# Optimization experiments

Hardware: AMD Instinct MI355X
Metric: run time of the kernel (lower is better)

Reference implementation:

```python
import jax, jax.numpy as jnp
import numpy as np

N = 100000        # num nodes
E2 = 3200000      # num directed edges (symmetric)
D = 256           # node feature dim
C = 40            # num classes
NIDS = 1000       # labelled node ids
TOL = 0.01
MAXITER = 16
AVG_DEG = E2 // N // 2 * 2  # ~32


def setup_inputs() -> dict:
    key = jax.random.key(0)
    k1, k2, k3, k4, k5, k6 = jax.random.split(key, 6)
    E = E2 // 2
    row_h = jax.random.randint(k1, (E,), 0, N, dtype=jnp.int32)
    col_h = jax.random.randint(k2, (E,), 0, N, dtype=jnp.int32)
    # symmetrize so I - (1-eps)*A is SPD-like (CG assumption)
    row = jnp.concatenate([row_h, col_h])
    col = jnp.concatenate([col_h, row_h])
    vals = jax.random.uniform(k3, (E,), dtype=jnp.float32) * (0.9 / 32.0)
    data = jnp.concatenate([vals, vals])
    node_features = jax.random.normal(k4, (N, D), dtype=jnp.float32)
    ids = jax.random.randint(k5, (NIDS,), 0, N, dtype=jnp.int32)
    # hk.Linear with TruncatedNormal(stddev=1/sqrt(D)) init
    W = (jax.random.truncated_normal(k6, -2.0, 2.0, (D, C), dtype=jnp.float32)
         * (1.0 / np.sqrt(D))).astype(jnp.float32)
    b = jnp.zeros((C,), jnp.float32)
    e0 = jnp.zeros((), jnp.float32)  # hk.get_parameter('e0', (), init=zeros)
    return dict(node_features=node_features, W=W, b=b, e0=e0,
                data=data, row=row, col=col, ids=ids)


def reference(node_features, W, b, e0, data, row, col, ids):
    epsilon = jax.nn.sigmoid(e0)
    # head_transform=None; d_feat > num_classes -> Linear first, then smooth
    x = node_features @ W + b  # [N, C]

    def spmv(v):  # adj @ v for COO adjacency, v: [N, C]
        return jax.ops.segment_sum(data[:, None] * v[col], row, num_segments=N)

    def f(v):  # (I - (1-eps) A) v
        return v - (1.0 - epsilon) * spmv(v)

    # smooth(): x.shape[1] (=C) <= ids.size -> direct CG on dense x, then gather ids
    sol, _ = jax.scipy.sparse.linalg.cg(f, x, tol=TOL, maxiter=MAXITER)
    return sol[ids]  # [NIDS, C] logits
```

## Files before the change

kernel.cpp:

```cpp
#include <hip/hip_runtime.h>
#include <hip/hip_fp16.h>
#include <math.h>

#define NNODE  100000
#define NEDGE  3200000
#define DFEAT  256
#define NCLS   40
#define NC_TOT 4000000
#define NIDS   1000
#define TOLSQ  1.0e-4f
#define MAXIT  16

#define SB 2048
#define SLOT8 500000
#define SPB8 245
#define XB 1024
#define VT 256
#define GR     128
#define GEMM_B 782

#define RB      128
#define NBUCK   782
#define BCAP    6144
#define SUBB    1024
#define NPB     800
#define EPB     4000

__device__ __forceinline__ float block_reduce_256(float v, float* red) {
  int tid = threadIdx.x;
  red[tid] = v;
  __syncthreads();
  #pragma unroll
  for (int off = 128; off > 0; off >>= 1) {
    if (tid < off) red[tid] += red[tid + off];
    __syncthreads();
  }
  float res = red[0];
  __syncthreads();
  return res;
}

__global__ void __launch_bounds__(256) k_pcount(const int* __restrict__ row,
                                                int* __restrict__ cntmat,
                                                int* __restrict__ total) {
  __shared__ int h[NBUCK];
  int tid = threadIdx.x, blk = blockIdx.x;
  for (int i = tid; i < NBUCK; i += 256) h[i] = 0;
  __syncthreads();
  int e0 = blk * EPB;
  for (int i = tid; i < EPB; i += 256) atomicAdd(&h[row[e0 + i] >> 7], 1);
  __syncthreads();
  for (int i = tid; i < NBUCK; i += 256) {
    int v = h[i];
    cntmat[blk * NBUCK + i] = v;
    if (v) atomicAdd(&total[i], v);
  }
}

__global__ void k_bscan2(const int* __restrict__ total, int* __restrict__ bptr) {
  __shared__ int s[1024];
  int tid = threadIdx.x;
  int v = (tid < NBUCK) ? total[tid] : 0;
  s[tid] = v;
  __syncthreads();
  for (int off = 1; off < 1024; off <<= 1) {
    int t = (tid >= off) ? s[tid - off] : 0;
    __syncthreads();
    s[tid] += t;
    __syncthreads();
  }
  if (tid < NBUCK) bptr[tid] = s[tid] - v;
  if (tid == 0) bptr[NBUCK] = NEDGE;
}

__global__ void __launch_bounds__(1024) k_colscan(int* __restrict__ cntmat,
                                                  const int* __restrict__ bptr) {
  __shared__ int s[1024];
  int b = blockIdx.x;
  int tid = threadIdx.x;
  int v = (tid < NPB) ? cntmat[tid * NBUCK + b] : 0;
  s[tid] = v;
  __syncthreads();
  for (int off = 1; off < 1024; off <<= 1) {
    int t = (tid >= off) ? s[tid - off] : 0;
    __syncthreads();
    s[tid] += t;
    __syncthreads();
  }
  if (tid < NPB) cntmat[tid * NBUCK + b] = bptr[b] + s[tid] - v;
}

__global__ void __launch_bounds__(512) k_ppart(const int* __restrict__ row,
    const int* __restrict__ col, const float* __restrict__ data,
    const int* __restrict__ offmat, uint2* __restrict__ bstage) {
  __shared__ int cnt[NBUCK];
  __shared__ int segs[NBUCK + 1];
  __shared__ int cur[NBUCK];
  __shared__ int goff[NBUCK];
  __shared__ int scp[512];
  __shared__ unsigned short bof[EPB];
  __shared__ uint2 pay[EPB];
  int tid = threadIdx.x, blk = blockIdx.x;
  int e0 = blk * EPB;

  for (int i = tid; i < NBUCK; i += 512) {
    cnt[i] = 0;
    goff[i] = offmat[blk * NBUCK + i];
  }
  __syncthreads();
  for (int i = tid; i < EPB; i += 512) atomicAdd(&cnt[row[e0 + i] >> 7], 1);
  __syncthreads();

  int t2 = tid * 2;
  int l0 = (t2 + 0 < NBUCK) ? cnt[t2 + 0] : 0;
  int l1 = (t2 + 1 < NBUCK) ? cnt[t2 + 1] : 0;
  int mysum = l0 + l1;
  scp[tid] = mysum;
  __syncthreads();
  for (int off = 1; off < 512; off <<= 1) {
    int t = (tid >= off) ? scp[tid - off] : 0;
    __syncthreads();
    scp[tid] += t;
    __syncthreads();
  }
  int base = scp[tid] - mysum;
  if (t2 + 0 <= NBUCK) segs[t2 + 0] = base;  base += l0;
  if (t2 + 1 <= NBUCK) segs[t2 + 1] = base;
  for (int i = tid; i < NBUCK; i += 512) cur[i] = 0;
  __syncthreads();

  for (int b = tid; b < NBUCK; b += 512) {
    int s1 = segs[b + 1];
    for (int i = segs[b]; i < s1; ++i) bof[i] = (unsigned short)b;
  }
  for (int i = tid; i < EPB; i += 512) {
    int rr = row[e0 + i];
    int b = rr >> 7;
    int rk = atomicAdd(&cur[b], 1);
    pay[segs[b] + rk] = make_uint2(((unsigned)(rr & (RB - 1)) << 17) | (unsigned)col[e0 + i],
                                   __float_as_uint(data[e0 + i]));
  }
  __syncthreads();
  for (int i = tid; i < EPB; i += 512) {
    int b = bof[i];
    bstage[goff[b] + (i - segs[b])] = pay[i];
  }
}

__global__ void __launch_bounds__(512) k_bbuild(const int* __restrict__ bptr,
    const uint2* __restrict__ bstage, int* __restrict__ rowptr,
    int2* __restrict__ csr) {
  __shared__ uint2 ebuf[BCAP];
  __shared__ int deg[SUBB];
  __shared__ int segs[SUBB];
  __shared__ int scp[512];
  int b = blockIdx.x;
  int s0 = bptr[b], s1 = bptr[b + 1];
  int n = s1 - s0;
  if (n > BCAP) n = BCAP;
  int tid = threadIdx.x;
  for (int i = tid; i < SUBB; i += 512) deg[i] = 0;
  __syncthreads();
  for (int i = tid; i < n; i += 512) {
    uint2 e = bstage[s0 + i];
    ebuf[i] = e;
    int key = (int)(e.x >> 17) * 8 + (int)((e.x & 0x1FFFF) >> 14);
    atomicAdd(&deg[key], 1);
  }
  __syncthreads();
  int t2 = tid * 2;
  int l0 = deg[t2 + 0], l1 = deg[t2 + 1];
  int mysum = l0 + l1;
  scp[tid] = mysum;
  __syncthreads();
  for (int off = 1; off < 512; off <<= 1) {
    int t = (tid >= off) ? scp[tid - off] : 0;
    __syncthreads();
    scp[tid] += t;
    __syncthreads();
  }
  int base = scp[tid] - mysum;
  segs[t2 + 0] = base;  base += l0;
  segs[t2 + 1] = base;
  __syncthreads();
  for (int i = tid; i < SUBB; i += 512) deg[i] = 0;
  if (tid < RB) {
    int grow = b * RB + tid;
    if (grow < NNODE) rowptr[grow] = s0 + segs[tid * 8];
  }
  if (b == 0 && tid == 0) rowptr[NNODE] = NEDGE;
  __syncthreads();
  for (int i = tid; i < n; i += 512) {
    uint2 e = ebuf[i];
    int col = (int)(e.x & 0x1FFFF);
    int key = (int)(e.x >> 17) * 8 + (col >> 14);
    int pos = atomicAdd(&deg[key], 1);
    csr[s0 + segs[key] + pos] = make_int2(col, (int)e.y);
  }
}

__global__ void __launch_bounds__(256) k_gemm(const float* __restrict__ feat,
    const float* __restrict__ W, const float* __restrict__ bias,
    float* __restrict__ r, float* __restrict__ p, __half* __restrict__ ph,
    float* __restrict__ part) {
  __shared__ float wtile[DFEAT * NCLS];
  __shared__ float red[256];
  int tid = threadIdx.x;
  int r0 = blockIdx.x * GR;
  int rl0 = (tid >> 2) * 2;
  int cbase = (tid & 3) * 10;
  float acc0[10], acc1[10];
  #pragma unroll
  for (int j = 0; j < 10; ++j) {
    float bv = bias[cbase + j];
    acc0[j] = bv;
    acc1[j] = bv;
  }

  #pragma unroll
  for (int it = 0; it < DFEAT * NCLS / 256; ++it)
    wtile[tid + it * 256] = W[tid + it * 256];
  __syncthreads();

  int g0 = r0 + rl0, g1 = g0 + 1;
  int g0c = (g0 < NNODE) ? g0 : NNODE - 1;
  int g1c = (g1 < NNODE) ? g1 : NNODE - 1;
  const float* f0p = feat + (size_t)g0c * DFEAT;
  const float* f1p = feat + (size_t)g1c * DFEAT;

  #pragma unroll 4
  for (int kq = 0; kq < DFEAT / 4; ++kq) {
    float4 f0 = *(const float4*)(f0p + kq * 4);
    float4 f1 = *(const float4*)(f1p + kq * 4);
    const float* w0 = &wtile[(kq * 4 + 0) * NCLS + cbase];
    const float* w1 = &wtile[(kq * 4 + 1) * NCLS + cbase];
    const float* w2 = &wtile[(kq * 4 + 2) * NCLS + cbase];
    const float* w3 = &wtile[(kq * 4 + 3) * NCLS + cbase];
    #pragma unroll
    for (int j = 0; j < 10; ++j) {
      float wa = w0[j], wb = w1[j], wc = w2[j], wd = w3[j];
      acc0[j] = fmaf(f0.x, wa, acc0[j]);
      acc0[j] = fmaf(f0.y, wb, acc0[j]);
      acc0[j] = fmaf(f0.z, wc, acc0[j]);
      acc0[j] = fmaf(f0.w, wd, acc0[j]);
      acc1[j] = fmaf(f1.x, wa, acc1[j]);
      acc1[j] = fmaf(f1.y, wb, acc1[j]);
      acc1[j] = fmaf(f1.z, wc, acc1[j]);
      acc1[j] = fmaf(f1.w, wd, acc1[j]);
    }
  }

  float local = 0.f;
  if (g0 < NNODE) {
    size_t b0 = (size_t)g0 * NCLS + cbase;
    #pragma unroll
    for (int j = 0; j < 10; ++j) {
      float a = acc0[j];
      r[b0 + j] = a; p[b0 + j] = a; ph[b0 + j] = __float2half(a);
      local = fmaf(a, a, local);
    }
  }
  if (g1 < NNODE) {
    size_t b1 = (size_t)g1 * NCLS + cbase;
    #pragma unroll
    for (int j = 0; j < 10; ++j) {
      float a = acc1[j];
      r[b1 + j] = a; p[b1 + j] = a; ph[b1 + j] = __float2half(a);
      local = fmaf(a, a, local);
    }
  }
  float tot = block_reduce_256(local, red);
  if (tid == 0) part[blockIdx.x] = tot;
}

__global__ void k_init_scal(const float* __restrict__ part, const float* __restrict__ e0,
                            float* __restrict__ scal) {
  __shared__ float red[256];
  float local = 0.f;
  for (int i = threadIdx.x; i < GEMM_B; i += 256) local += part[i];
  float bs = block_reduce_256(local, red);
  if (threadIdx.x == 0) {
    float eps = 1.f / (1.f + expf(-e0[0]));
    scal[0] = 1.f - eps;
    scal[1] = TOLSQ * bs;
    scal[2] = bs;
  }
}

__global__ void __launch_bounds__(VT) k_spmv(const float* __restrict__ scal, int k,
    const int* __restrict__ rowptr, const int2* __restrict__ csr,
    const __half* __restrict__ ph, const float* __restrict__ p,
    float* __restrict__ Ap, float* __restrict__ part) {
  float gamma = scal[2 + k], atol2 = scal[1];
  if (!(gamma > atol2)) return;
  float omega = scal[0];
  int b = blockIdx.x;
  int chunk = (b & 7) * (SB / 8) + (b >> 3);
  int sbase = chunk * SPB8;
  float local = 0.f;
  int li = threadIdx.x;
  int s = sbase + li;
  if (li < SPB8 && s < SLOT8) {
    int rr = s / 5;
    int c8 = (s - rr * 5) * 8;
    int s0 = rowptr[rr], s1 = rowptr[rr + 1];
    float a0 = 0.f, a1 = 0.f, a2 = 0.f, a3 = 0.f;
    float a4 = 0.f, a5 = 0.f, a6 = 0.f, a7 = 0.f;
    #pragma unroll 4
    for (int j = s0; j < s1; ++j) {
      int2 pr = csr[j];
      float w = __int_as_float(pr.y);
      uint4 g = *(const uint4*)(ph + (size_t)pr.x * NCLS + c8);
      float2 f01 = __half22float2(*(__half2*)&g.x);
      float2 f23 = __half22float2(*(__half2*)&g.y);
      float2 f45 = __half22float2(*(__half2*)&g.z);
      float2 f67 = __half22float2(*(__half2*)&g.w);
      a0 = fmaf(w, f01.x, a0); a1 = fmaf(w, f01.y, a1);
      a2 = fmaf(w, f23.x, a2); a3 = fmaf(w, f23.y, a3);
      a4 = fmaf(w, f45.x, a4); a5 = fmaf(w, f45.y, a5);
      a6 = fmaf(w, f67.x, a6); a7 = fmaf(w, f67.y, a7);
    }
    size_t e = (size_t)rr * NCLS + c8;
    float4 pe0 = *(const float4*)(p + e);
    float4 pe1 = *(const float4*)(p + e + 4);
    float4 v0, v1;
    v0.x = fmaf(-omega, a0, pe0.x); v0.y = fmaf(-omega, a1, pe0.y);
    v0.z = fmaf(-omega, a2, pe0.z); v0.w = fmaf(-omega, a3, pe0.w);
    v1.x = fmaf(-omega, a4, pe1.x); v1.y = fmaf(-omega, a5, pe1.y);
    v1.z = fmaf(-omega, a6, pe1.z); v1.w = fmaf(-omega, a7, pe1.w);
    *(float4*)(Ap + e) = v0;
    *(float4*)(Ap + e + 4) = v1;
    local = fmaf(pe0.x, v0.x, local); local = fmaf(pe0.y, v0.y, local);
    local = fmaf(pe0.z, v0.z, local); local = fmaf(pe0.w, v0.w, local);
    local = fmaf(pe1.x, v1.x, local); local = fmaf(pe1.y, v1.y, local);
    local = fmaf(pe1.z, v1.z, local); local = fmaf(pe1.w, v1.w, local);
  }
  __shared__ float red[256];
  float tot = block_reduce_256(local, red);
  if (threadIdx.x == 0) part[blockIdx.x] = tot;
}

__global__ void __launch_bounds__(VT) k_xr(const float* __restrict__ scal, int k,
    const float* __restrict__ part_in,
    const float* __restrict__ p, const float* __restrict__ Ap,
    float* __restrict__ r, const int* __restrict__ ids,
    float* __restrict__ out, float* __restrict__ part_out) {
  float gamma = scal[2 + k], atol2 = scal[1];
  if (!(gamma > atol2)) return;
  __shared__ float red[256];
  float lp = 0.f;
  for (int i = threadIdx.x; i < SB; i += VT) lp += part_in[i];
  float pap = block_reduce_256(lp, red);
  float alpha = gamma / pap;
  int idx = blockIdx.x * VT + threadIdx.x;
  if (idx < NIDS * NCLS) {
    int i = idx / NCLS, c = idx - (idx / NCLS) * NCLS;
    out[idx] += alpha * p[(size_t)ids[i] * NCLS + c];
  }
  const float4* a4 = (const float4*)Ap;
  float4* r4 = (float4*)r;
  float local = 0.f;
  int stride = gridDim.x * blockDim.x;
  for (int e = blockIdx.x * blockDim.x + threadIdx.x; e < NC_TOT / 4; e += stride) {
    float4 ae = a4[e], re = r4[e];
    re.x = fmaf(-alpha, ae.x, re.x); re.y = fmaf(-alpha, ae.y, re.y);
    re.z = fmaf(-alpha, ae.z, re.z); re.w = fmaf(-alpha, ae.w, re.w);
    r4[e] = re;
    local = fmaf(re.x, re.x, local); local = fmaf(re.y, re.y, local);
    local = fmaf(re.z, re.z, local); local = fmaf(re.w, re.w, local);
  }
  float tot = block_reduce_256(local, red);
  if (threadIdx.x == 0) part_out[blockIdx.x] = tot;
}

__global__ void __launch_bounds__(VT) k_pupd(float* __restrict__ scal, int k,
    const float* __restrict__ part_in,
    const float* __restrict__ r, float* __restrict__ p, __half* __restrict__ ph) {
  float gamma = scal[2 + k], atol2 = scal[1];
  if (!(gamma > atol2)) {
    if (blockIdx.x == 0 && threadIdx.x == 0) scal[2 + k + 1] = gamma;
    return;
  }
  __shared__ float red[256];
  float lp = 0.f;
  for (int i = threadIdx.x; i < XB; i += VT) lp += part_in[i];
  float gnew = block_reduce_256(lp, red);
  float beta = gnew / gamma;
  const float4* r4 = (const float4*)r;
  float4* p4 = (float4*)p;
  int stride = gridDim.x * blockDim.x;
  for (int e = blockIdx.x * blockDim.x + threadIdx.x; e < NC_TOT / 4; e += stride) {
    float4 pe = p4[e], re = r4[e];
    pe.x = fmaf(beta, pe.x, re.x); pe.y = fmaf(beta, pe.y, re.y);
    pe.z = fmaf(beta, pe.z, re.z); pe.w = fmaf(beta, pe.w, re.w);
    p4[e] = pe;
    int e4 = e * 4;
    ph[e4 + 0] = __float2half(pe.x);
    ph[e4 + 1] = __float2half(pe.y);
    ph[e4 + 2] = __float2half(pe.z);
    ph[e4 + 3] = __float2half(pe.w);
  }
  if (blockIdx.x == 0 && threadIdx.x == 0) scal[2 + k + 1] = gnew;
}

extern "C" void kernel_launch(void* const* d_in, const int* in_sizes, int n_in,
                              void* d_out, int out_size, void* d_ws, size_t ws_size,
                              hipStream_t stream) {
  const float* feat = (const float*)d_in[0];
  const float* W    = (const float*)d_in[1];
  const float* bias = (const float*)d_in[2];
  const float* e0   = (const float*)d_in[3];
  const float* data = (const float*)d_in[4];
  const int*   row  = (const int*)d_in[5];
  const int*   col  = (const int*)d_in[6];
  const int*   ids  = (const int*)d_in[7];
  float* out = (float*)d_out;

  size_t off = 0;
  char* base = (char*)d_ws;
  auto take = [&](size_t nbytes) -> void* {
    void* ptr = base + off;
    off += (nbytes + 255) & ~(size_t)255;
    return ptr;
  };
  float* rv  = (float*)take((size_t)NC_TOT * 4);
  float* pv  = (float*)take((size_t)NC_TOT * 4);
  float* ap  = (float*)take((size_t)NC_TOT * 4);
  __half* ph = (__half*)take((size_t)NC_TOT * 2);
  int2*  csr = (int2*)take((size_t)NEDGE * 8);
  int* rowptr    = (int*)take((size_t)(NNODE + 1) * 4);
  int* cntmat    = (int*)take((size_t)NPB * NBUCK * 4);
  int* total     = (int*)take((size_t)(NBUCK + 2) * 4);
  int* bptr      = (int*)take((size_t)(NBUCK + 2) * 4);
  float* part_a  = (float*)take(SB * 4);
  float* part_b  = (float*)take(XB * 4);
  float* scal    = (float*)take(64 * 4);

  uint2* bstage = (uint2*)rv;

  hipMemsetAsync(total, 0, (size_t)(NBUCK + 2) * 4, stream);
  hipMemsetAsync(out, 0, (size_t)NIDS * NCLS * 4, stream);
  k_pcount<<<NPB, 256, 0, stream>>>(row, cntmat, total);
  k_bscan2<<<1, 1024, 0, stream>>>(total, bptr);
  k_colscan<<<NBUCK, 1024, 0, stream>>>(cntmat, bptr);
  k_ppart<<<NPB, 512, 0, stream>>>(row, col, data, cntmat, bstage);
  k_bbuild<<<NBUCK, 512, 0, stream>>>(bptr, bstage, rowptr, csr);

  k_gemm<<<GEMM_B, 256, 0, stream>>>(feat, W, bias, rv, pv, ph, part_a);
  k_init_scal<<<1, 256, 0, stream>>>(part_a, e0, scal);

  for (int k = 0; k < MAXIT; ++k) {
    k_spmv<<<SB, VT, 0, stream>>>(scal, k, rowptr, csr, ph, pv, ap, part_a);
    k_xr  <<<XB, VT, 0, stream>>>(scal, k, part_a, pv, ap, rv, ids, out, part_b);
    k_pupd<<<XB, VT, 0, stream>>>(scal, k, part_b, rv, pv, ph);
  }
}
```

Measured before the change: 389.7 us.

## Split GEMM reduction dimension across two blocks and combine in a separate kernel

The feature-projection GEMM now splits the 256-wide reduction into two halves handled by separate blocks. This doubles the grid and halves the shared W tile, which should raise occupancy. A new combine kernel adds the two partial results, writes r, p and the half-precision p, and computes the initial residual norm partials. The cost is an extra 16MB partial buffer and an additional kernel pass over 4M-element arrays.

```diff
diff --git a/kernel.cpp b/kernel.cpp
--- a/kernel.cpp
+++ b/kernel.cpp
@@ -18,6 +18,8 @@
 #define VT 256
 #define GR     128
 #define GEMM_B 782
+#define GEMM_B2 1564
+#define KHALF  128
 
 #define RB      128
 #define NBUCK   782
@@ -201,35 +203,35 @@
 
 __global__ void __launch_bounds__(256) k_gemm(const float* __restrict__ feat,
     const float* __restrict__ W, const float* __restrict__ bias,
-    float* __restrict__ r, float* __restrict__ p, __half* __restrict__ ph,
-    float* __restrict__ part) {
-  __shared__ float wtile[DFEAT * NCLS];
-  __shared__ float red[256];
+    float* __restrict__ pb0, float* __restrict__ pb1) {
+  __shared__ float wtile[KHALF * NCLS];
   int tid = threadIdx.x;
-  int r0 = blockIdx.x * GR;
+  int b = blockIdx.x;
+  int half = b & 1;
+  int r0 = (b >> 1) * GR;
   int rl0 = (tid >> 2) * 2;
   int cbase = (tid & 3) * 10;
   float acc0[10], acc1[10];
   #pragma unroll
   for (int j = 0; j < 10; ++j) {
-    float bv = bias[cbase + j];
+    float bv = half ? 0.f : bias[cbase + j];
     acc0[j] = bv;
     acc1[j] = bv;
   }
 
   #pragma unroll
-  for (int it = 0; it < DFEAT * NCLS / 256; ++it)
-    wtile[tid + it * 256] = W[tid + it * 256];
+  for (int it = 0; it < KHALF * NCLS / 256; ++it)
+    wtile[tid + it * 256] = W[half * KHALF * NCLS + tid + it * 256];
   __syncthreads();
 
   int g0 = r0 + rl0, g1 = g0 + 1;
   int g0c = (g0 < NNODE) ? g0 : NNODE - 1;
   int g1c = (g1 < NNODE) ? g1 : NNODE - 1;
-  const float* f0p = feat + (size_t)g0c * DFEAT;
-  const float* f1p = feat + (size_t)g1c * DFEAT;
+  const float* f0p = feat + (size_t)g0c * DFEAT + half * KHALF;
+  const float* f1p = feat + (size_t)g1c * DFEAT + half * KHALF;
 
   #pragma unroll 4
-  for (int kq = 0; kq < DFEAT / 4; ++kq) {
+  for (int kq = 0; kq < KHALF / 4; ++kq) {
     float4 f0 = *(const float4*)(f0p + kq * 4);
     float4 f1 = *(const float4*)(f1p + kq * 4);
     const float* w0 = &wtile[(kq * 4 + 0) * NCLS + cbase];
@@ -250,34 +252,52 @@
     }
   }
 
-  float local = 0.f;
+  float* __restrict__ pb = half ? pb1 : pb0;
   if (g0 < NNODE) {
     size_t b0 = (size_t)g0 * NCLS + cbase;
     #pragma unroll
-    for (int j = 0; j < 10; ++j) {
-      float a = acc0[j];
-      r[b0 + j] = a; p[b0 + j] = a; ph[b0 + j] = __float2half(a);
-      local = fmaf(a, a, local);
-    }
+    for (int j = 0; j < 10; ++j) pb[b0 + j] = acc0[j];
   }
   if (g1 < NNODE) {
     size_t b1 = (size_t)g1 * NCLS + cbase;
     #pragma unroll
-    for (int j = 0; j < 10; ++j) {
-      float a = acc1[j];
-      r[b1 + j] = a; p[b1 + j] = a; ph[b1 + j] = __float2half(a);
-      local = fmaf(a, a, local);
-    }
+    for (int j = 0; j < 10; ++j) pb[b1 + j] = acc1[j];
+  }
+}
+
+__global__ void __launch_bounds__(VT) k_gcomb(const float* __restrict__ pb0,
+    const float* __restrict__ pb1, float* __restrict__ r, float* __restrict__ p,
+    __half* __restrict__ ph, float* __restrict__ part) {
+  __shared__ float red[256];
+  const float4* a4 = (const float4*)pb0;
+  const float4* b4 = (const float4*)pb1;
+  float4* r4 = (float4*)r;
+  float4* p4 = (float4*)p;
+  float local = 0.f;
+  int stride = gridDim.x * blockDim.x;
+  for (int e = blockIdx.x * blockDim.x + threadIdx.x; e < NC_TOT / 4; e += stride) {
+    float4 a = a4[e], b = b4[e];
+    float4 v;
+    v.x = a.x + b.x; v.y = a.y + b.y; v.z = a.z + b.z; v.w = a.w + b.w;
+    r4[e] = v; p4[e] = v;
+    __half2 h01 = __floats2half2_rn(v.x, v.y);
+    __half2 h23 = __floats2half2_rn(v.z, v.w);
+    uint2 pack;
+    pack.x = *(unsigned*)&h01;
+    pack.y = *(unsigned*)&h23;
+    *(uint2*)(ph + (size_t)e * 4) = pack;
+    local = fmaf(v.x, v.x, local); local = fmaf(v.y, v.y, local);
+    local = fmaf(v.z, v.z, local); local = fmaf(v.w, v.w, local);
   }
   float tot = block_reduce_256(local, red);
-  if (tid == 0) part[blockIdx.x] = tot;
+  if (threadIdx.x == 0) part[blockIdx.x] = tot;
 }
 
 __global__ void k_init_scal(const float* __restrict__ part, const float* __restrict__ e0,
                             float* __restrict__ scal) {
   __shared__ float red[256];
   float local = 0.f;
-  for (int i = threadIdx.x; i < GEMM_B; i += 256) local += part[i];
+  for (int i = threadIdx.x; i < XB; i += 256) local += part[i];
   float bs = block_reduce_256(local, red);
   if (threadIdx.x == 0) {
     float eps = 1.f / (1.f + expf(-e0[0]));
@@ -426,6 +446,7 @@
   float* rv  = (float*)take((size_t)NC_TOT * 4);
   float* pv  = (float*)take((size_t)NC_TOT * 4);
   float* ap  = (float*)take((size_t)NC_TOT * 4);
+  float* pb1 = (float*)take((size_t)NC_TOT * 4);
   __half* ph = (__half*)take((size_t)NC_TOT * 2);
   int2*  csr = (int2*)take((size_t)NEDGE * 8);
   int* rowptr    = (int*)take((size_t)(NNODE + 1) * 4);
@@ -437,6 +458,7 @@
   float* scal    = (float*)take(64 * 4);
 
   uint2* bstage = (uint2*)rv;
+  float* pb0 = ap;
 
   hipMemsetAsync(total, 0, (size_t)(NBUCK + 2) * 4, stream);
   hipMemsetAsync(out, 0, (size_t)NIDS * NCLS * 4, stream);
@@ -446,8 +468,9 @@
   k_ppart<<<NPB, 512, 0, stream>>>(row, col, data, cntmat, bstage);
   k_bbuild<<<NBUCK, 512, 0, stream>>>(bptr, bstage, rowptr, csr);
 
-  k_gemm<<<GEMM_B, 256, 0, stream>>>(feat, W, bias, rv, pv, ph, part_a);
-  k_init_scal<<<1, 256, 0, stream>>>(part_a, e0, scal);
+  k_gemm<<<GEMM_B2, 256, 0, stream>>>(feat, W, bias, pb0, pb1);
+  k_gcomb<<<XB, VT, 0, stream>>>(pb0, pb1, rv, pv, ph, part_b);
+  k_init_scal<<<1, 256, 0, stream>>>(part_b, e0, scal);
 
   for (int k = 0; k < MAXIT; ++k) {
     k_spmv<<<SB, VT, 0, stream>>>(scal, k, rowptr, csr, ph, pv, ap, part_a);
```

Measured after the change: 406.8 us. 1.04x slower.
